# Optimization experiments

Measured on AMD Instinct MI355X. Metric: run time of the kernel, lower is better.

## Reference

```python
import jax, jax.numpy as jnp
import numpy as np
import math

B, N, D, H = 4, 2048, 512, 8
DK = D // H


def setup_inputs() -> dict:
    key = jax.random.key(0)
    ks = jax.random.split(key, 7)
    s = 1.0 / math.sqrt(D)
    return {
        "Q": jax.random.normal(ks[0], (B, N, D), jnp.float32),
        "K": jax.random.normal(ks[1], (B, N, D), jnp.float32),
        "V": jax.random.normal(ks[2], (B, N, D), jnp.float32),
        "Wq": jax.random.normal(ks[3], (D, D), jnp.float32) * s,
        "bq": jax.random.normal(ks[4], (D,), jnp.float32) * s,
        "Wo": jax.random.normal(ks[5], (D, D), jnp.float32) * s,
        "bo": jax.random.normal(ks[6], (D,), jnp.float32) * s,
    }


def _split_heads(x):
    b, n, _ = x.shape
    return x.reshape(b, n, H, DK).transpose(0, 2, 1, 3)  # [B,H,N,dk]


def reference(Q, K, V, Wq, bq, Wo, bo):
    # Faithful to source: W_q projects Q, K, AND V (source bug kept).
    proj = lambda x: jnp.einsum("bnd,ed->bne", x, Wq) + bq
    q = _split_heads(proj(Q))
    k = _split_heads(proj(K))
    v = _split_heads(proj(V))
    scores = jnp.einsum("bhnd,bhmd->bhnm", q, k) / math.sqrt(DK)  # [B,H,N,N]
    # Faithful to source: softmax over dim=1 == the HEADS axis.
    probs = jax.nn.softmax(scores, axis=1)
    A = jnp.einsum("bhnm,bhmd->bhnd", probs, v)  # [B,H,N,dk]
    A = A.transpose(0, 2, 1, 3).reshape(B, N, D)  # combine heads
    return jnp.einsum("bnd,ed->bne", A, Wo) + bo
```

## Files before the change

kernel.cpp:

```cpp
#include <hip/hip_runtime.h>
#include <hip/hip_bf16.h>

#define B_  4
#define N_  2048
#define D_  512
#define H_  8

typedef unsigned short u16;
typedef __attribute__((ext_vector_type(8))) unsigned short ushort8;
typedef __attribute__((ext_vector_type(4))) unsigned short us4;
typedef __attribute__((ext_vector_type(8))) short short8;
typedef __attribute__((ext_vector_type(4))) float float4v;

__device__ __forceinline__ float bf2f(u16 u) {
    union { unsigned int i; float f; } v;
    v.i = ((unsigned int)u) << 16;
    return v.f;
}
__device__ __forceinline__ u16 f2bf(float f) {
    union { float f; unsigned int i; } v;
    v.f = f;
    unsigned int r = v.i + 0x7FFFu + ((v.i >> 16) & 1u);
    return (u16)(r >> 16);
}
__device__ __forceinline__ u16 f2bf_fast(float f) {
    union { float f; unsigned int i; } v;
    v.f = f;
    return (u16)((v.i + 0x8000u) >> 16);
}

__device__ __forceinline__ void gload_lds16(const void* g, void* l) {
    __builtin_amdgcn_global_load_lds(
        (const __attribute__((address_space(1))) unsigned int*)g,
        (__attribute__((address_space(3))) unsigned int*)l, 16, 0, 0);
}

#define WAIT_VM(N) do { \
    asm volatile("s_waitcnt vmcnt(" #N ")" ::: "memory"); \
    __builtin_amdgcn_sched_barrier(0); } while (0)
#define WAIT_LGKM0 do { \
    asm volatile("s_waitcnt lgkmcnt(0)" ::: "memory"); \
    __builtin_amdgcn_sched_barrier(0); } while (0)
#define BARRIER do { \
    __builtin_amdgcn_s_barrier(); \
    __builtin_amdgcn_sched_barrier(0); } while (0)

__global__ __launch_bounds__(256) void wconv(
    const float* __restrict__ Wq, const float* __restrict__ Wo,
    u16* __restrict__ out)
{
    const int idx = (blockIdx.x * 256 + threadIdx.x) * 8;
    const float* src = blockIdx.y ? Wo : Wq;
    u16* dst = out + (size_t)blockIdx.y * (D_ * D_) + idx;
    float4v a = *(const float4v*)(src + idx);
    float4v b = *(const float4v*)(src + idx + 4);
    ushort8 o;
    #pragma unroll
    for (int j = 0; j < 4; ++j) { o[j] = f2bf(a[j]); o[j + 4] = f2bf(b[j]); }
    *(ushort8*)dst = o;
}

__global__ __launch_bounds__(256) void proj1_mfma(
    const float* __restrict__ X0, const float* __restrict__ X1,
    const float* __restrict__ X2, const u16* __restrict__ Wb,
    const float* __restrict__ bias, u16* __restrict__ C0)
{
    __shared__ u16 As[128][32];
    __shared__ u16 Bs[128][32];

    const int t = threadIdx.x;
    const int flat = blockIdx.x;
    const int xcd = flat & 7, rr = flat >> 3;
    const int eb = rr & 3, g = rr >> 2;
    const int zm = xcd + 8 * g;
    const int z  = zm >> 6;
    const int e0 = eb * 128;
    const int m0 = (zm & 63) * 128;

    const float* X = (z == 0) ? X0 : ((z == 1) ? X1 : X2);
    const int w = t >> 6, l = t & 63;
    const int lane16 = l & 15, quad = l >> 4;
    const int wr = (w >> 1) * 64;
    const int wc = (w & 1) * 64;

    float4v acc[4][4];
    #pragma unroll
    for (int i = 0; i < 4; ++i)
        #pragma unroll
        for (int j = 0; j < 4; ++j)
            acc[i][j] = (float4v){0.f, 0.f, 0.f, 0.f};

    for (int k0 = 0; k0 < 512; k0 += 32) {
        __syncthreads();

        #pragma unroll
        for (int i = 0; i < 2; ++i) {
            int v   = t + 256 * i;
            int row = v >> 2;
            int c8  = (v & 3) * 8;
            const float* xp = X + (size_t)(m0 + row) * 512 + k0 + c8;
            float4v x0 = *(const float4v*)xp;
            float4v x1 = *(const float4v*)(xp + 4);
            ushort8 o;
            #pragma unroll
            for (int j = 0; j < 4; ++j) {
                o[j]     = f2bf_fast(x0[j]);
                o[j + 4] = f2bf_fast(x1[j]);
            }
            *(ushort8*)&As[row][c8] = o;
        }

        #pragma unroll
        for (int i = 0; i < 2; ++i) {
            int r0 = w * 32 + i * 16;
            gload_lds16(Wb + (size_t)(e0 + r0 + (l >> 2)) * 512 + k0 + (l & 3) * 8,
                        &Bs[r0][0]);
        }
        __syncthreads();

        short8 af[4], bfr[4];
        #pragma unroll
        for (int i = 0; i < 4; ++i)
            af[i] = *(const short8*)&As[wr + i * 16 + lane16][quad * 8];
        #pragma unroll
        for (int j = 0; j < 4; ++j)
            bfr[j] = *(const short8*)&Bs[wc + j * 16 + lane16][quad * 8];
        #pragma unroll
        for (int i = 0; i < 4; ++i)
            #pragma unroll
            for (int j = 0; j < 4; ++j)
                acc[i][j] = __builtin_amdgcn_mfma_f32_16x16x32_bf16(
                    af[i], bfr[j], acc[i][j], 0, 0, 0);
    }

    float bj[4];
    #pragma unroll
    for (int j = 0; j < 4; ++j) bj[j] = bias[e0 + wc + j * 16 + lane16];

    if (z == 2) {
        u16* C = C0 + 2 * (size_t)B_ * N_ * D_;
        #pragma unroll
        for (int i = 0; i < 4; ++i) {
            int mrow = m0 + wr + i * 16 + quad * 4;
            int bb = mrow >> 11, nb = mrow & (N_ - 1);
            #pragma unroll
            for (int j = 0; j < 4; ++j) {
                int e = e0 + wc + j * 16 + lane16;
                us4 o;
                #pragma unroll
                for (int r = 0; r < 4; ++r) o[r] = f2bf(acc[i][j][r] + bj[j]);
                *(us4*)(C + (size_t)(bb * D_ + e) * N_ + nb) = o;
            }
        }
    } else {
        u16* C = C0 + (size_t)z * (size_t)B_ * N_ * D_;
        #pragma unroll
        for (int i = 0; i < 4; ++i)
            #pragma unroll
            for (int j = 0; j < 4; ++j) {
                int e = e0 + wc + j * 16 + lane16;
                #pragma unroll
                for (int r = 0; r < 4; ++r) {
                    int mrow = m0 + wr + i * 16 + quad * 4 + r;
                    C[(size_t)mrow * D_ + e] = f2bf(acc[i][j][r] + bj[j]);
                }
            }
    }
}

__global__ __launch_bounds__(256) void proj2_mfma(
    const u16* __restrict__ P0, const u16* __restrict__ P1,
    const u16* __restrict__ Wv, const float* __restrict__ bias,
    float* __restrict__ C)
{
    __shared__ u16 As[128][32];
    __shared__ u16 Bs[64][32];

    const int t = threadIdx.x;
    const int flat = blockIdx.x;
    const int xcd = flat & 7, rr = flat >> 3;
    const int eb = rr & 7, g = rr >> 3;
    const int m0 = (xcd + 8 * g) * 128;
    const int e0 = eb * 64;

    const int w = t >> 6, l = t & 63;
    const int lane16 = l & 15, quad = l >> 4;
    const int wr = (w >> 1) * 64;
    const int wc = (w & 1) * 32;

    float4v acc[4][2];
    #pragma unroll
    for (int i = 0; i < 4; ++i)
        #pragma unroll
        for (int j = 0; j < 2; ++j)
            acc[i][j] = (float4v){0.f, 0.f, 0.f, 0.f};

    for (int k0 = 0; k0 < 512; k0 += 32) {
        __syncthreads();

        #pragma unroll
        for (int i = 0; i < 2; ++i) {
            int v   = t + 256 * i;
            int row = v >> 2;
            int c8  = (v & 3) * 8;
            size_t gi = (size_t)(m0 + row) * 512 + k0 + c8;
            ushort8 a = *(const ushort8*)(P0 + gi);
            ushort8 b = *(const ushort8*)(P1 + gi);
            ushort8 o;
            #pragma unroll
            for (int j = 0; j < 8; ++j) o[j] = f2bf(bf2f(a[j]) + bf2f(b[j]));
            *(ushort8*)&As[row][c8] = o;
        }

        gload_lds16(Wv + (size_t)(e0 + w * 16 + (l >> 2)) * 512 + k0 + (l & 3) * 8,
                    &Bs[w * 16][0]);
        __syncthreads();

        short8 af[4], bfr[2];
        #pragma unroll
        for (int i = 0; i < 4; ++i)
            af[i] = *(const short8*)&As[wr + i * 16 + lane16][quad * 8];
        #pragma unroll
        for (int j = 0; j < 2; ++j)
            bfr[j] = *(const short8*)&Bs[wc + j * 16 + lane16][quad * 8];
        #pragma unroll
        for (int i = 0; i < 4; ++i)
            #pragma unroll
            for (int j = 0; j < 2; ++j)
                acc[i][j] = __builtin_amdgcn_mfma_f32_16x16x32_bf16(
                    af[i], bfr[j], acc[i][j], 0, 0, 0);
    }

    float bj[2];
    #pragma unroll
    for (int j = 0; j < 2; ++j) bj[j] = bias[e0 + wc + j * 16 + lane16];

    #pragma unroll
    for (int i = 0; i < 4; ++i)
        #pragma unroll
        for (int j = 0; j < 2; ++j) {
            int e = e0 + wc + j * 16 + lane16;
            #pragma unroll
            for (int r = 0; r < 4; ++r) {
                int mrow = m0 + wr + i * 16 + quad * 4 + r;
                C[(size_t)mrow * D_ + e] = acc[i][j][r] + bj[j];
            }
        }
}

__global__ __launch_bounds__(512, 2) void attn_mfma6(
    const u16* __restrict__ Qp, const u16* __restrict__ Kp,
    const u16* __restrict__ Vpt, u16* __restrict__ A0)
{
    __shared__ u16 Ks[2][32][520];
    __shared__ u16 Vs[512][36];
    __shared__ u16 Ps[4][8][16][36];

    const int t = threadIdx.x;
    const int w = t >> 6, l = t & 63;
    const int lane16 = l & 15, quad = l >> 4;
    const int ns = w >> 1, ms = w & 1;

    const int flat = blockIdx.x;
    const int xcd  = flat & 7;
    const int b = xcd >> 1;
    const int z = xcd & 1;
    const int n0 = (flat >> 3) * 64 + ns * 16;
    const int seg  = N_ / 2;
    const int mbeg = z * seg;
    u16* A = A0 + (size_t)z * ((size_t)B_ * N_ * D_);

    const u16* Kb = Kp + (size_t)b * N_ * D_;
    const int vd0 = t >> 2, vpart = (t & 3) * 8;
    const u16* Vsrc = Vpt + (size_t)(b * D_) * N_ + vpart;

    short8 qfrag[8][2];
    {
        const u16* qb = Qp + ((size_t)(b * N_ + n0 + lane16) * D_ + quad * 8);
        #pragma unroll
        for (int h = 0; h < 8; ++h)
            #pragma unroll
            for (int dc = 0; dc < 2; ++dc)
                qfrag[h][dc] = *(const short8*)(qb + h * 64 + dc * 32);
    }

    float4v aacc[8][2];
    #pragma unroll
    for (int h = 0; h < 8; ++h)
        #pragma unroll
        for (int dt = 0; dt < 2; ++dt)
            aacc[h][dt] = (float4v){0.f, 0.f, 0.f, 0.f};

    ushort8 vreg[4];
    const int nch = seg / 32;

    #pragma unroll
    for (int i = 0; i < 4; ++i)
        gload_lds16(Kb + (size_t)(mbeg + w * 4 + i) * D_ + l * 8,
                    &Ks[0][w * 4 + i][0]);
    #pragma unroll
    for (int i = 0; i < 4; ++i)
        vreg[i] = *(const ushort8*)(Vsrc + (size_t)(i * 128 + vd0) * N_ + mbeg);
    #pragma unroll
    for (int i = 0; i < 4; ++i)
        gload_lds16(Kb + (size_t)(mbeg + 32 + w * 4 + i) * D_ + l * 8,
                    &Ks[1][w * 4 + i][0]);
    WAIT_VM(8);
    BARRIER;

    for (int c = 0; c < nch; ++c) {
        const int cur = c & 1;
        const int mc  = mbeg + c * 32;

        if (c < nch - 1) { WAIT_VM(4); } else { WAIT_VM(0); }

        #pragma unroll
        for (int i = 0; i < 4; ++i)
            *(ushort8*)&Vs[i * 128 + vd0][vpart] = vreg[i];

        float4v sacc[8];
        #pragma unroll
        for (int h = 0; h < 8; ++h) sacc[h] = (float4v){0.f, 0.f, 0.f, 0.f};
        __builtin_amdgcn_s_setprio(1);
        #pragma unroll
        for (int h = 0; h < 8; ++h)
            #pragma unroll
            for (int dc = 0; dc < 2; ++dc) {
                short8 kf = *(const short8*)
                    &Ks[cur][ms * 16 + lane16][h * 64 + dc * 32 + quad * 8];
                sacc[h] = __builtin_amdgcn_mfma_f32_16x16x32_bf16(
                    qfrag[h][dc], kf, sacc[h], 0, 0, 0);
            }
        __builtin_amdgcn_s_setprio(0);

        #pragma unroll
        for (int r = 0; r < 4; ++r) {
            float p[8]; float sum = 0.f;
            #pragma unroll
            for (int h = 0; h < 8; ++h) {
                p[h] = __expf(sacc[h][r] * 0.125f);
                sum += p[h];
            }
            float inv = __builtin_amdgcn_rcpf(sum);
            #pragma unroll
            for (int h = 0; h < 8; ++h)
                Ps[ns][h][quad * 4 + r][ms * 16 + lane16] = f2bf_fast(p[h] * inv);
        }

        if (c + 1 < nch) {
            #pragma unroll
            for (int i = 0; i < 4; ++i)
                vreg[i] = *(const ushort8*)
                    (Vsrc + (size_t)(i * 128 + vd0) * N_ + mc + 32);
        }

        WAIT_LGKM0;
        BARRIER;

        if (c + 2 < nch) {
            #pragma unroll
            for (int i = 0; i < 4; ++i)
                gload_lds16(Kb + (size_t)(mc + 64 + w * 4 + i) * D_ + l * 8,
                            &Ks[cur][w * 4 + i][0]);
        }

        __builtin_amdgcn_s_setprio(1);
        #pragma unroll
        for (int h = 0; h < 8; ++h) {
            short8 pf = *(const short8*)&Ps[ns][h][lane16][quad * 8];
            #pragma unroll
            for (int dt = 0; dt < 2; ++dt) {
                short8 vf = *(const short8*)
                    &Vs[h * 64 + (ms * 2 + dt) * 16 + lane16][quad * 8];
                aacc[h][dt] = __builtin_amdgcn_mfma_f32_16x16x32_bf16(
                    pf, vf, aacc[h][dt], 0, 0, 0);
            }
        }
        __builtin_amdgcn_s_setprio(0);

        if (c < nch - 1) {
            if (c + 2 < nch) { WAIT_VM(8); } else { WAIT_VM(4); }
            WAIT_LGKM0;
            BARRIER;
        }
    }

    #pragma unroll
    for (int h = 0; h < 8; ++h)
        #pragma unroll
        for (int dt = 0; dt < 2; ++dt)
            #pragma unroll
            for (int r = 0; r < 4; ++r) {
                const int n = n0 + quad * 4 + r;
                const int d = h * 64 + (ms * 2 + dt) * 16 + lane16;
                A[(size_t)(b * N_ + n) * D_ + d] = f2bf(aacc[h][dt][r]);
            }
}

extern "C" void kernel_launch(void* const* d_in, const int* in_sizes, int n_in,
                              void* d_out, int out_size, void* d_ws, size_t ws_size,
                              hipStream_t stream)
{
    const float* Q  = (const float*)d_in[0];
    const float* K  = (const float*)d_in[1];
    const float* V  = (const float*)d_in[2];
    const float* Wq = (const float*)d_in[3];
    const float* bq = (const float*)d_in[4];
    const float* Wo = (const float*)d_in[5];
    const float* bo = (const float*)d_in[6];
    float* out = (float*)d_out;
    u16*   ws  = (u16*)d_ws;

    const size_t NBD = (size_t)B_ * N_ * D_;

    u16* Qp  = ws;
    u16* Kp  = ws + NBD;
    u16* Vpt = ws + 2 * NBD;
    u16* Pa  = ws + 3 * NBD;
    u16* Pb  = ws + 4 * NBD;
    u16* Wb  = ws + 5 * NBD;

    wconv<<<dim3(128, 2), dim3(256), 0, stream>>>(Wq, Wo, Wb);

    proj1_mfma<<<dim3(768), dim3(256), 0, stream>>>(
        Q, K, V, Wb, bq, Qp);

    attn_mfma6<<<dim3(256), dim3(512), 0, stream>>>(Qp, Kp, Vpt, Pa);

    proj2_mfma<<<dim3(512), dim3(256), 0, stream>>>(
        Pa, Pb, Wb + (size_t)D_ * D_, bo, out);
}
```

Before: 240.6 us.

## Pre-convert inputs to bf16 and software-pipeline projection GEMMs with multi-buffered LDS

Adds a conversion kernel that turns Q/K/V and both weight matrices into bf16 in a larger workspace. The Q/K/V projection then streams both operands into LDS with direct global-to-LDS loads, using a triple-buffered pipeline and wait counters in place of full syncthreads. The fp32 fallback projection and the output projection get double buffering with register prefetch, plus priority hints around the MFMA bursts. The aim is to hide global-load latency behind MFMA work. The cost is an extra full pass writing bf16 copies of the inputs and more LDS per block, and the new path only runs when the workspace is large enough.

New measurement: 224.5 us. -6.7%, faster.

```diff
diff --git a/kernel.cpp b/kernel.cpp
--- a/kernel.cpp
+++ b/kernel.cpp
@@ -60,13 +60,84 @@
     *(ushort8*)dst = o;
 }
 
-__global__ __launch_bounds__(256) void proj1_mfma(
-    const float* __restrict__ X0, const float* __restrict__ X1,
-    const float* __restrict__ X2, const u16* __restrict__ Wb,
+__global__ __launch_bounds__(256) void cvt4(
+    const float* __restrict__ Q, const float* __restrict__ K,
+    const float* __restrict__ V, const float* __restrict__ Wq,
+    const float* __restrict__ Wo, u16* __restrict__ out,
+    u16* __restrict__ wb)
+{
+    const int y = blockIdx.y;
+    if (y == 3) {
+        if (blockIdx.x >= 256) return;
+        const int idx = (blockIdx.x * 256 + threadIdx.x) * 8;
+        const bool hi = idx >= D_ * D_;
+        const float* src = hi ? Wo : Wq;
+        const int off = hi ? idx - D_ * D_ : idx;
+        float4v a = *(const float4v*)(src + off);
+        float4v b = *(const float4v*)(src + off + 4);
+        ushort8 o;
+        #pragma unroll
+        for (int j = 0; j < 4; ++j) { o[j] = f2bf(a[j]); o[j + 4] = f2bf(b[j]); }
+        *(ushort8*)(wb + idx) = o;
+        return;
+    }
+    const size_t NBD = (size_t)B_ * N_ * D_;
+    const float* src = (y == 0) ? Q : ((y == 1) ? K : V);
+    u16* dst = out + (size_t)y * NBD;
+    size_t idx = ((size_t)blockIdx.x * 256 + threadIdx.x) * 8;
+    float4v a = *(const float4v*)(src + idx);
+    float4v b = *(const float4v*)(src + idx + 4);
+    ushort8 o;
+    #pragma unroll
+    for (int j = 0; j < 4; ++j) { o[j] = f2bf(a[j]); o[j + 4] = f2bf(b[j]); }
+    *(ushort8*)(dst + idx) = o;
+}
+
+__device__ __forceinline__ void proj1_store(
+    float4v (&acc)[4][4], const float* bias, u16* C0,
+    int z, int m0, int e0, int wr, int wc, int lane16, int quad)
+{
+    float bj[4];
+    #pragma unroll
+    for (int j = 0; j < 4; ++j) bj[j] = bias[e0 + wc + j * 16 + lane16];
+
+    if (z == 2) {
+        u16* C = C0 + 2 * (size_t)B_ * N_ * D_;
+        #pragma unroll
+        for (int i = 0; i < 4; ++i) {
+            int mrow = m0 + wr + i * 16 + quad * 4;
+            int bb = mrow >> 11, nb = mrow & (N_ - 1);
+            #pragma unroll
+            for (int j = 0; j < 4; ++j) {
+                int e = e0 + wc + j * 16 + lane16;
+                us4 o;
+                #pragma unroll
+                for (int r = 0; r < 4; ++r) o[r] = f2bf(acc[i][j][r] + bj[j]);
+                *(us4*)(C + (size_t)(bb * D_ + e) * N_ + nb) = o;
+            }
+        }
+    } else {
+        u16* C = C0 + (size_t)z * (size_t)B_ * N_ * D_;
+        #pragma unroll
+        for (int i = 0; i < 4; ++i)
+            #pragma unroll
+            for (int j = 0; j < 4; ++j) {
+                int e = e0 + wc + j * 16 + lane16;
+                #pragma unroll
+                for (int r = 0; r < 4; ++r) {
+                    int mrow = m0 + wr + i * 16 + quad * 4 + r;
+                    C[(size_t)mrow * D_ + e] = f2bf(acc[i][j][r] + bj[j]);
+                }
+            }
+    }
+}
+
+__global__ __launch_bounds__(256) void proj1g(
+    const u16* __restrict__ Xb, const u16* __restrict__ Wb,
     const float* __restrict__ bias, u16* __restrict__ C0)
 {
-    __shared__ u16 As[128][32];
-    __shared__ u16 Bs[128][32];
+    __shared__ u16 As[3][128][32];
+    __shared__ u16 Bs[3][128][32];
 
     const int t = threadIdx.x;
     const int flat = blockIdx.x;
@@ -77,11 +148,93 @@
     const int e0 = eb * 128;
     const int m0 = (zm & 63) * 128;
 
+    const u16* X = Xb + (size_t)z * ((size_t)B_ * N_ * D_);
+    const int w = t >> 6, l = t & 63;
+    const int lane16 = l & 15, quad = l >> 4;
+    const int wr = (w >> 1) * 64;
+    const int wc = (w & 1) * 64;
+
+    const int arow = l >> 2, acol = (l & 3) * 8;
+
+    float4v acc[4][4];
+    #pragma unroll
+    for (int i = 0; i < 4; ++i)
+        #pragma unroll
+        for (int j = 0; j < 4; ++j)
+            acc[i][j] = (float4v){0.f, 0.f, 0.f, 0.f};
+
+#define P1_STAGE(buf, k0) do { \
+        _Pragma("unroll") \
+        for (int i = 0; i < 2; ++i) { \
+            int r0 = w * 32 + i * 16; \
+            gload_lds16(X + (size_t)(m0 + r0 + arow) * 512 + (k0) + acol, \
+                        &As[buf][r0][0]); \
+        } \
+        _Pragma("unroll") \
+        for (int i = 0; i < 2; ++i) { \
+            int r0 = w * 32 + i * 16; \
+            gload_lds16(Wb + (size_t)(e0 + r0 + arow) * 512 + (k0) + acol, \
+                        &Bs[buf][r0][0]); \
+        } } while (0)
+
+    P1_STAGE(0, 0);
+    P1_STAGE(1, 32);
+
+    #pragma unroll
+    for (int c = 0; c < 16; ++c) {
+        const int cur = c % 3;
+        if (c < 15) { WAIT_VM(4); } else { WAIT_VM(0); }
+        BARRIER;
+
+        short8 af[4], bfr[4];
+        #pragma unroll
+        for (int i = 0; i < 4; ++i)
+            af[i] = *(const short8*)&As[cur][wr + i * 16 + lane16][quad * 8];
+        #pragma unroll
+        for (int j = 0; j < 4; ++j)
+            bfr[j] = *(const short8*)&Bs[cur][wc + j * 16 + lane16][quad * 8];
+
+        if (c + 2 < 16) P1_STAGE((c + 2) % 3, (c + 2) * 32);
+
+        __builtin_amdgcn_s_setprio(1);
+        #pragma unroll
+        for (int i = 0; i < 4; ++i)
+            #pragma unroll
+            for (int j = 0; j < 4; ++j)
+                acc[i][j] = __builtin_amdgcn_mfma_f32_16x16x32_bf16(
+                    af[i], bfr[j], acc[i][j], 0, 0, 0);
+        __builtin_amdgcn_s_setprio(0);
+    }
+#undef P1_STAGE
+
+    proj1_store(acc, bias, C0, z, m0, e0, wr, wc, lane16, quad);
+}
+
+__global__ __launch_bounds__(256) void proj1f(
+    const float* __restrict__ X0, const float* __restrict__ X1,
+    const float* __restrict__ X2, const u16* __restrict__ Wb,
+    const float* __restrict__ bias, u16* __restrict__ C0)
+{
+    __shared__ u16 As[2][128][32];
+    __shared__ u16 Bs[2][128][32];
+
+    const int t = threadIdx.x;
+    const int flat = blockIdx.x;
+    const int xcd = flat & 7, rr = flat >> 3;
+    const int eb = rr & 3, g = rr >> 2;
+    const int zm = xcd + 8 * g;
+    const int z  = zm >> 6;
+    const int e0 = eb * 128;
+    const int m0 = (zm & 63) * 128;
+
     const float* X = (z == 0) ? X0 : ((z == 1) ? X1 : X2);
     const int w = t >> 6, l = t & 63;
     const int lane16 = l & 15, quad = l >> 4;
     const int wr = (w >> 1) * 64;
     const int wc = (w & 1) * 64;
+    const int arow = l >> 2, acol = (l & 3) * 8;
+
+    const int xrow = t >> 2, xc8 = (t & 3) * 8;
 
     float4v acc[4][4];
     #pragma unroll
@@ -90,91 +243,80 @@
         for (int j = 0; j < 4; ++j)
             acc[i][j] = (float4v){0.f, 0.f, 0.f, 0.f};
 
-    for (int k0 = 0; k0 < 512; k0 += 32) {
-        __syncthreads();
+    float4v xr[2][2][2];
+
+#define P1F_LOADA(k0) do { \
+        _Pragma("unroll") \
+        for (int i = 0; i < 2; ++i) { \
+            const float* xp = X + (size_t)(m0 + xrow + i * 64) * 512 + (k0) + xc8; \
+            xr[i][0][0] = *(const float4v*)xp; \
+            xr[i][0][1] = *(const float4v*)(xp + 4); \
+        } } while (0)
+
+#define P1F_STAGEB(buf, k0) do { \
+        _Pragma("unroll") \
+        for (int i = 0; i < 2; ++i) { \
+            int r0 = w * 32 + i * 16; \
+            gload_lds16(Wb + (size_t)(e0 + r0 + arow) * 512 + (k0) + acol, \
+                        &Bs[buf][r0][0]); \
+        } } while (0)
+
+    P1F_LOADA(0);
+    P1F_STAGEB(0, 0);
+
+    #pragma unroll
+    for (int c = 0; c < 16; ++c) {
+        const int cur = c & 1;
+        WAIT_VM(0);
 
         #pragma unroll
         for (int i = 0; i < 2; ++i) {
-            int v   = t + 256 * i;
-            int row = v >> 2;
-            int c8  = (v & 3) * 8;
-            const float* xp = X + (size_t)(m0 + row) * 512 + k0 + c8;
-            float4v x0 = *(const float4v*)xp;
-            float4v x1 = *(const float4v*)(xp + 4);
             ushort8 o;
             #pragma unroll
             for (int j = 0; j < 4; ++j) {
-                o[j]     = f2bf_fast(x0[j]);
-                o[j + 4] = f2bf_fast(x1[j]);
-            }
-            *(ushort8*)&As[row][c8] = o;
-        }
-
-        #pragma unroll
-        for (int i = 0; i < 2; ++i) {
-            int r0 = w * 32 + i * 16;
-            gload_lds16(Wb + (size_t)(e0 + r0 + (l >> 2)) * 512 + k0 + (l & 3) * 8,
-                        &Bs[r0][0]);
-        }
-        __syncthreads();
+                o[j]     = f2bf_fast(xr[i][0][0][j]);
+                o[j + 4] = f2bf_fast(xr[i][0][1][j]);
+            }
+            *(ushort8*)&As[cur][xrow + i * 64][xc8] = o;
+        }
+        WAIT_LGKM0;
+        BARRIER;
 
         short8 af[4], bfr[4];
         #pragma unroll
         for (int i = 0; i < 4; ++i)
-            af[i] = *(const short8*)&As[wr + i * 16 + lane16][quad * 8];
+            af[i] = *(const short8*)&As[cur][wr + i * 16 + lane16][quad * 8];
         #pragma unroll
         for (int j = 0; j < 4; ++j)
-            bfr[j] = *(const short8*)&Bs[wc + j * 16 + lane16][quad * 8];
+            bfr[j] = *(const short8*)&Bs[cur][wc + j * 16 + lane16][quad * 8];
+
+        if (c + 1 < 16) {
+            P1F_LOADA((c + 1) * 32);
+            P1F_STAGEB(cur ^ 1, (c + 1) * 32);
+        }
+
+        __builtin_amdgcn_s_setprio(1);
         #pragma unroll
         for (int i = 0; i < 4; ++i)
             #pragma unroll
             for (int j = 0; j < 4; ++j)
                 acc[i][j] = __builtin_amdgcn_mfma_f32_16x16x32_bf16(
                     af[i], bfr[j], acc[i][j], 0, 0, 0);
-    }
-
-    float bj[4];
-    #pragma unroll
-    for (int j = 0; j < 4; ++j) bj[j] = bias[e0 + wc + j * 16 + lane16];
-
-    if (z == 2) {
-        u16* C = C0 + 2 * (size_t)B_ * N_ * D_;
-        #pragma unroll
-        for (int i = 0; i < 4; ++i) {
-            int mrow = m0 + wr + i * 16 + quad * 4;
-            int bb = mrow >> 11, nb = mrow & (N_ - 1);
-            #pragma unroll
-            for (int j = 0; j < 4; ++j) {
-                int e = e0 + wc + j * 16 + lane16;
-                us4 o;
-                #pragma unroll
-                for (int r = 0; r < 4; ++r) o[r] = f2bf(acc[i][j][r] + bj[j]);
-                *(us4*)(C + (size_t)(bb * D_ + e) * N_ + nb) = o;
-            }
-        }
-    } else {
-        u16* C = C0 + (size_t)z * (size_t)B_ * N_ * D_;
-        #pragma unroll
-        for (int i = 0; i < 4; ++i)
-            #pragma unroll
-            for (int j = 0; j < 4; ++j) {
-                int e = e0 + wc + j * 16 + lane16;
-                #pragma unroll
-                for (int r = 0; r < 4; ++r) {
-                    int mrow = m0 + wr + i * 16 + quad * 4 + r;
-                    C[(size_t)mrow * D_ + e] = f2bf(acc[i][j][r] + bj[j]);
-                }
-            }
-    }
-}
-
-__global__ __launch_bounds__(256) void proj2_mfma(
+        __builtin_amdgcn_s_setprio(0);
+    }
+#undef P1F_LOADA
+#undef P1F_STAGEB
+
+    proj1_store(acc, bias, C0, z, m0, e0, wr, wc, lane16, quad);
+}
+
+__global__ __launch_bounds__(256) void proj2p(
     const u16* __restrict__ P0, const u16* __restrict__ P1,
     const u16* __restrict__ Wv, const float* __restrict__ bias,
     float* __restrict__ C)
 {
-    __shared__ u16 As[128][32];
-    __shared__ u16 Bs[64][32];
+    __shared__ u16 As[2][128][32];
+    __shared__ u16 Bs[2][64][32];
 
     const int t = threadIdx.x;
     const int flat = blockIdx.x;
@@ -187,6 +329,8 @@
     const int lane16 = l & 15, quad = l >> 4;
     const int wr = (w >> 1) * 64;
     const int wc = (w & 1) * 32;
+    const int arow = l >> 2, acol = (l & 3) * 8;
+    const int xrow = t >> 2, xc8 = (t & 3) * 8;
 
     float4v acc[4][2];
     #pragma unroll
@@ -195,41 +339,59 @@
         for (int j = 0; j < 2; ++j)
             acc[i][j] = (float4v){0.f, 0.f, 0.f, 0.f};
 
-    for (int k0 = 0; k0 < 512; k0 += 32) {
-        __syncthreads();
+    ushort8 pa[2], pb[2];
+
+#define P2_LOADP(k0) do { \
+        _Pragma("unroll") \
+        for (int i = 0; i < 2; ++i) { \
+            size_t gi = (size_t)(m0 + xrow + i * 64) * 512 + (k0) + xc8; \
+            pa[i] = *(const ushort8*)(P0 + gi); \
+            pb[i] = *(const ushort8*)(P1 + gi); \
+        } } while (0)
+
+    P2_LOADP(0);
+    gload_lds16(Wv + (size_t)(e0 + w * 16 + arow) * 512 + 0 + acol, &Bs[0][w * 16][0]);
+
+    #pragma unroll
+    for (int c = 0; c < 16; ++c) {
+        const int cur = c & 1;
+        WAIT_VM(0);
 
         #pragma unroll
         for (int i = 0; i < 2; ++i) {
-            int v   = t + 256 * i;
-            int row = v >> 2;
-            int c8  = (v & 3) * 8;
-            size_t gi = (size_t)(m0 + row) * 512 + k0 + c8;
-            ushort8 a = *(const ushort8*)(P0 + gi);
-            ushort8 b = *(const ushort8*)(P1 + gi);
             ushort8 o;
             #pragma unroll
-            for (int j = 0; j < 8; ++j) o[j] = f2bf(bf2f(a[j]) + bf2f(b[j]));
-            *(ushort8*)&As[row][c8] = o;
-        }
-
-        gload_lds16(Wv + (size_t)(e0 + w * 16 + (l >> 2)) * 512 + k0 + (l & 3) * 8,
-                    &Bs[w * 16][0]);
-        __syncthreads();
+            for (int j = 0; j < 8; ++j)
+                o[j] = f2bf(bf2f(pa[i][j]) + bf2f(pb[i][j]));
+            *(ushort8*)&As[cur][xrow + i * 64][xc8] = o;
+        }
+        WAIT_LGKM0;
+        BARRIER;
 
         short8 af[4], bfr[2];
         #pragma unroll
         for (int i = 0; i < 4; ++i)
-            af[i] = *(const short8*)&As[wr + i * 16 + lane16][quad * 8];
+            af[i] = *(const short8*)&As[cur][wr + i * 16 + lane16][quad * 8];
         #pragma unroll
         for (int j = 0; j < 2; ++j)
-            bfr[j] = *(const short8*)&Bs[wc + j * 16 + lane16][quad * 8];
+            bfr[j] = *(const short8*)&Bs[cur][wc + j * 16 + lane16][quad * 8];
+
+        if (c + 1 < 16) {
+            P2_LOADP((c + 1) * 32);
+            gload_lds16(Wv + (size_t)(e0 + w * 16 + arow) * 512 + (c + 1) * 32 + acol,
+                        &Bs[cur ^ 1][w * 16][0]);
+        }
+
+        __builtin_amdgcn_s_setprio(1);
         #pragma unroll
         for (int i = 0; i < 4; ++i)
             #pragma unroll
             for (int j = 0; j < 2; ++j)
                 acc[i][j] = __builtin_amdgcn_mfma_f32_16x16x32_bf16(
                     af[i], bfr[j], acc[i][j], 0, 0, 0);
-    }
+        __builtin_amdgcn_s_setprio(0);
+    }
+#undef P2_LOADP
 
     float bj[2];
     #pragma unroll
@@ -413,20 +575,39 @@
 
     const size_t NBD = (size_t)B_ * N_ * D_;
 
-    u16* Qp  = ws;
-    u16* Kp  = ws + NBD;
-    u16* Vpt = ws + 2 * NBD;
-    u16* Pa  = ws + 3 * NBD;
-    u16* Pb  = ws + 4 * NBD;
-    u16* Wb  = ws + 5 * NBD;
-
-    wconv<<<dim3(128, 2), dim3(256), 0, stream>>>(Wq, Wo, Wb);
-
-    proj1_mfma<<<dim3(768), dim3(256), 0, stream>>>(
-        Q, K, V, Wb, bq, Qp);
-
-    attn_mfma6<<<dim3(256), dim3(512), 0, stream>>>(Qp, Kp, Vpt, Pa);
-
-    proj2_mfma<<<dim3(512), dim3(256), 0, stream>>>(
-        Pa, Pb, Wb + (size_t)D_ * D_, bo, out);
-}
+    const size_t need6 = (6 * NBD + 2 * (size_t)D_ * D_) * sizeof(u16);
+
+    if (ws_size >= need6) {
+        u16* S0 = ws;
+        u16* S1 = ws + NBD;
+        u16* S3 = ws + 3 * NBD;
+        u16* Wb = ws + 6 * NBD;
+
+        cvt4<<<dim3((unsigned)(NBD / 2048), 4), dim3(256), 0, stream>>>(
+            Q, K, V, Wq, Wo, S0, Wb);
+
+        proj1g<<<dim3(768), dim3(256), 0, stream>>>(S0, Wb, bq, S3);
+
+        attn_mfma6<<<dim3(256), dim3(512), 0, stream>>>(
+            S3, S3 + NBD, S3 + 2 * NBD, S0);
+
+        proj2p<<<dim3(512), dim3(256), 0, stream>>>(
+            S0, S1, Wb + (size_t)D_ * D_, bo, out);
+    } else {
+        u16* Qp  = ws;
+        u16* Kp  = ws + NBD;
+        u16* Vpt = ws + 2 * NBD;
+        u16* Pa  = ws + 3 * NBD;
+        u16* Pb  = ws + 4 * NBD;
+        u16* Wb  = ws + 5 * NBD;
+
+        wconv<<<dim3(128, 2), dim3(256), 0, stream>>>(Wq, Wo, Wb);
+
+        proj1f<<<dim3(768), dim3(256), 0, stream>>>(Q, K, V, Wb, bq, Qp);
+
+        attn_mfma6<<<dim3(256), dim3(512), 0, stream>>>(Qp, Kp, Vpt, Pa);
+
+        proj2p<<<dim3(512), dim3(256), 0, stream>>>(
+            Pa, Pb, Wb + (size_t)D_ * D_, bo, out);
+    }
+}
```
